# Kernel optimization log

Hardware: AMD Instinct MI355X
Metric: run time of the kernel (lower is better)

## Reference

```python
import jax, jax.numpy as jnp
import numpy as np

N_NODES = 50000
N_EDGES = 800000
T_SEQ = 2048
H = 128  # LSTM hidden size


def _lstm_dir(x, w_ih, w_hh, b, reverse):
    # x: [T, Din]; torch gate order: i, f, g, o
    xg = x @ w_ih.T + b  # [T, 4H] precomputed input contribution
    h0 = jnp.zeros((H,), x.dtype)

    def step(carry, g_t):
        h, c = carry
        g = g_t + h @ w_hh.T
        i, f, gg, o = jnp.split(g, 4)
        i = jax.nn.sigmoid(i); f = jax.nn.sigmoid(f)
        gg = jnp.tanh(gg); o = jax.nn.sigmoid(o)
        c = f * c + i * gg
        h = o * jnp.tanh(c)
        return (h, c), h

    _, hs = jax.lax.scan(step, (h0, h0), xg, reverse=reverse)
    return hs  # [T, H], time-aligned with x


def _bilstm(x, layer_params):
    for (wif, whf, bf, wir, whr, br) in layer_params:
        hf = _lstm_dir(x, wif, whf, bf, reverse=False)
        hr = _lstm_dir(x, wir, whr, br, reverse=True)
        x = jnp.concatenate([hf, hr], axis=-1)
    return x  # [T, 2H]


def _forward(g_mol, feat_seq, edge_src, edge_dst, edge_weight, smiles_kmer,
             w_ih_l0, w_hh_l0, b_ih_l0, b_hh_l0,
             w_ih_l0_r, w_hh_l0_r, b_ih_l0_r, b_hh_l0_r,
             w_ih_l1, w_hh_l1, b_ih_l1, b_hh_l1,
             w_ih_l1_r, w_hh_l1_r, b_ih_l1_r, b_hh_l1_r,
             W1, b1, W2, b2,
             fc1_w, fc1_b, fc2_w, fc2_b, fc3_w, fc3_b, fc4_w, fc4_b):
    n = feat_seq.shape[0]
    # ---- BiLSTM encoder over the (unbatched) molecule sequence [T,17] ----
    layer_params = [
        (w_ih_l0, w_hh_l0, b_ih_l0 + b_hh_l0, w_ih_l0_r, w_hh_l0_r, b_ih_l0_r + b_hh_l0_r),
        (w_ih_l1, w_hh_l1, b_ih_l1 + b_hh_l1, w_ih_l1_r, w_hh_l1_r, b_ih_l1_r + b_hh_l1_r),
    ]
    lstm_out = _bilstm(g_mol, layer_params)              # [T, 256]
    g_mol_vec = lstm_out.mean(axis=0, keepdims=True)     # [1, 256] (mean over dim 0, keepdim)

    # ---- GraphConv 1 (norm='none'): weighted sum-aggregate src->dst, then linear ----
    msg = edge_weight[:, None] * feat_seq[edge_src]                # [E, 128]
    agg = jax.ops.segment_sum(msg, edge_dst, num_segments=n)      # [N, 128]
    h = jax.nn.relu(agg @ W1 + b1)
    # ---- GraphConv 2 ----
    msg2 = edge_weight[:, None] * h[edge_src]                      # [E, 128]
    agg2 = jax.ops.segment_sum(msg2, edge_dst, num_segments=n)    # [N, 128]
    h2 = agg2 @ W2 + b2                                            # [N, 256]
    hg_seq = h2.mean(axis=0, keepdims=True)                        # [1, 256] single-graph mean_nodes

    # ---- concat + MLP head ----
    features = jnp.concatenate([hg_seq, g_mol_vec, smiles_kmer], axis=1)  # [1, 1150]
    out = jax.nn.relu(features @ fc1_w.T + fc1_b)
    out = jax.nn.relu(out @ fc2_w.T + fc2_b)
    out = jax.nn.relu(out @ fc3_w.T + fc3_b)
    out = out @ fc4_w.T + fc4_b
    return out  # [1, 1]


def setup_inputs():
    key = jax.random.key(0)
    ks = iter(jax.random.split(key, 48))

    def rn(shape, s=0.05):
        return jax.random.normal(next(ks), shape, dtype=jnp.float32) * s

    inp = {}
    inp["g_mol"] = jax.random.normal(next(ks), (T_SEQ, 17), dtype=jnp.float32)
    inp["feat_seq"] = jax.random.normal(next(ks), (N_NODES, 128), dtype=jnp.float32)
    inp["edge_src"] = jax.random.randint(next(ks), (N_EDGES,), 0, N_NODES)
    inp["edge_dst"] = jax.random.randint(next(ks), (N_EDGES,), 0, N_NODES)
    inp["edge_weight"] = jax.random.uniform(next(ks), (N_EDGES,), dtype=jnp.float32)
    inp["smiles_kmer"] = jax.random.normal(next(ks), (1, 638), dtype=jnp.float32)
    for l, din in ((0, 17), (1, 2 * H)):
        for suf in ("", "_r"):
            inp[f"w_ih_l{l}{suf}"] = rn((4 * H, din))
            inp[f"w_hh_l{l}{suf}"] = rn((4 * H, H))
            inp[f"b_ih_l{l}{suf}"] = rn((4 * H,))
            inp[f"b_hh_l{l}{suf}"] = rn((4 * H,))
    inp["W1"] = rn((128, 128)); inp["b1"] = jnp.zeros((128,), jnp.float32)
    inp["W2"] = rn((128, 256)); inp["b2"] = jnp.zeros((256,), jnp.float32)
    inp["fc1_w"] = rn((575, 1150)); inp["fc1_b"] = jnp.zeros((575,), jnp.float32)
    inp["fc2_w"] = rn((256, 575)); inp["fc2_b"] = jnp.zeros((256,), jnp.float32)
    inp["fc3_w"] = rn((64, 256)); inp["fc3_b"] = jnp.zeros((64,), jnp.float32)
    inp["fc4_w"] = rn((1, 64)); inp["fc4_b"] = jnp.zeros((1,), jnp.float32)
    return inp


def reference(g_mol, feat_seq, edge_src, edge_dst, edge_weight, smiles_kmer,
              w_ih_l0, w_hh_l0, b_ih_l0, b_hh_l0,
              w_ih_l0_r, w_hh_l0_r, b_ih_l0_r, b_hh_l0_r,
              w_ih_l1, w_hh_l1, b_ih_l1, b_hh_l1,
              w_ih_l1_r, w_hh_l1_r, b_ih_l1_r, b_hh_l1_r,
              W1, b1, W2, b2,
              fc1_w, fc1_b, fc2_w, fc2_b, fc3_w, fc3_b, fc4_w, fc4_b):
    return _forward(g_mol, feat_seq, edge_src, edge_dst, edge_weight, smiles_kmer,
                    w_ih_l0, w_hh_l0, b_ih_l0, b_hh_l0,
                    w_ih_l0_r, w_hh_l0_r, b_ih_l0_r, b_hh_l0_r,
                    w_ih_l1, w_hh_l1, b_ih_l1, b_hh_l1,
                    w_ih_l1_r, w_hh_l1_r, b_ih_l1_r, b_hh_l1_r,
                    W1, b1, W2, b2,
                    fc1_w, fc1_b, fc2_w, fc2_b, fc3_w, fc3_b, fc4_w, fc4_b)
```

## Files before the change

### kernel.cpp

```cpp
#include <hip/hip_runtime.h>
#include <hip/hip_bf16.h>

#define T_SEQ 2048
#define HID 128
#define G4 512
#define N_NODES 50000
#define N_EDGES 800000

typedef float f32x4 __attribute__((ext_vector_type(4)));
typedef _Float16 f16x2 __attribute__((ext_vector_type(2)));
typedef _Float16 f16x8 __attribute__((ext_vector_type(8)));

__device__ __forceinline__ float fast_sigmoid(float x) {
    return 1.0f / (1.0f + __expf(-x));
}
__device__ __forceinline__ float fast_tanh(float x) {
    return 1.0f - 2.0f / (__expf(2.0f * x) + 1.0f);
}

__device__ __forceinline__ float dot2_f16(float bits_w, f16x2 h2, float acc) {
    f16x2 w2 = __builtin_bit_cast(f16x2, bits_w);
#if __has_builtin(__builtin_amdgcn_fdot2)
    return __builtin_amdgcn_fdot2(w2, h2, acc, false);
#else
    asm("v_dot2_f32_f16 %0, %1, %2, %0" : "+v"(acc) : "v"(w2), "v"(h2));
    return acc;
#endif
}

__global__ void xg0_kernel(const float* __restrict__ g_mol,
                           const float* __restrict__ wf, const float* __restrict__ bfi, const float* __restrict__ bfh,
                           const float* __restrict__ wr, const float* __restrict__ bri, const float* __restrict__ brh,
                           float* __restrict__ xg_f, float* __restrict__ xg_r)
{
    int gid = blockIdx.x * blockDim.x + threadIdx.x;
    int j = gid & (G4 - 1);
    int rest = gid >> 9;
    int t = rest & (T_SEQ - 1);
    int dir = rest >> 11;
    const float* w  = dir ? wr  : wf;
    const float* bi = dir ? bri : bfi;
    const float* bh = dir ? brh : bfh;
    float* xg = dir ? xg_r : xg_f;
    const float* x  = g_mol + t * 17;
    const float* wj = w + j * 17;
    float acc = bi[j] + bh[j];
    #pragma unroll
    for (int k = 0; k < 17; ++k) acc += x[k] * wj[k];
    xg[t * G4 + j] = acc;
}

#define EDGE_BLOCKS ((N_EDGES + 1023) / 1024)
__global__ void hist_kernel(const int* __restrict__ esrc, const int* __restrict__ edst,
                            const float* __restrict__ ew,
                            int* __restrict__ cnt, float* __restrict__ outw)
{
    int e = blockIdx.x * 1024 + threadIdx.x;
    if (e < N_EDGES) {
        atomicAdd(&cnt[edst[e]], 1);
        atomicAdd(&outw[esrc[e]], ew[e]);
    }
}

__global__ __launch_bounds__(1024)
void prefix_kernel(const int* __restrict__ cnt, int* __restrict__ offs, int* __restrict__ cursor)
{
    __shared__ int part[1024];
    const int tid = threadIdx.x;
    const int CH = (N_NODES + 1023) / 1024;
    int base = tid * CH;
    int sum = 0;
    for (int i = 0; i < CH; ++i) { int idx = base + i; if (idx < N_NODES) sum += cnt[idx]; }
    part[tid] = sum;
    __syncthreads();
    for (int d = 1; d < 1024; d <<= 1) {
        int v = (tid >= d) ? part[tid - d] : 0;
        __syncthreads();
        part[tid] += v;
        __syncthreads();
    }
    int run = (tid == 0) ? 0 : part[tid - 1];
    for (int i = 0; i < CH; ++i) {
        int idx = base + i;
        if (idx < N_NODES) { offs[idx] = run; cursor[idx] = run; run += cnt[idx]; }
    }
    if (tid == 1023) offs[N_NODES] = run;
}

__global__ void reorder_kernel(const int* __restrict__ esrc, const int* __restrict__ edst,
                               const float* __restrict__ ew, int* __restrict__ cursor,
                               int* __restrict__ csr_src, float* __restrict__ csr_w)
{
    int e = blockIdx.x * 1024 + threadIdx.x;
    if (e < N_EDGES) {
        int pos = atomicAdd(&cursor[edst[e]], 1);
        csr_src[pos] = esrc[e];
        csr_w[pos]   = ew[e];
    }
}

struct ScanSmem {
    _Float16 h16[2][HID] __attribute__((aligned(16)));
    float g[G4];
    float part[G4];
};

#define B8(M) M(0,0,1,2,3) M(1,4,5,6,7) M(2,8,9,10,11) M(3,12,13,14,15) \
              M(4,16,17,18,19) M(5,20,21,22,23) M(6,24,25,26,27) M(7,28,29,30,31)
#define P32(M) M(0) M(1) M(2) M(3) M(4) M(5) M(6) M(7) M(8) M(9) M(10) M(11) \
               M(12) M(13) M(14) M(15) M(16) M(17) M(18) M(19) M(20) M(21) M(22) \
               M(23) M(24) M(25) M(26) M(27) M(28) M(29) M(30) M(31)

__device__ __forceinline__ void lstm_scan_dev(ScanSmem* sm, int dir,
                                              const float* __restrict__ xg,
                                              const float* __restrict__ whh,
                                              float* __restrict__ out,
                                              float* __restrict__ gvec, int write_out)
{
    const int tid = threadIdx.x;
    const int j = tid & (G4 - 1);
    const int half = tid >> 9;

    const float* wptr = whh + j * HID + half * 64;

#define DECL_PK(p) float apk##p; { \
    f16x2 pk_ = { (_Float16)wptr[2*(p)], (_Float16)wptr[2*(p)+1] }; \
    float bits_ = __builtin_bit_cast(float, pk_); \
    asm volatile("v_accvgpr_write_b32 %0, %1" : "=a"(apk##p) : "v"(bits_)); }
    P32(DECL_PK)
#undef DECL_PK

    if (tid < HID) sm->h16[0][tid] = (_Float16)0.0f;
    float c = 0.0f;
    float msum = 0.0f;
    __syncthreads();

    int t0 = dir ? (T_SEQ - 1) : 0;
    float xv = (half == 0) ? xg[t0 * G4 + j] : 0.0f;

    int pp = 0;
    for (int s = 0; s < T_SEQ; ++s) {
        int s2 = (s + 1 < T_SEQ) ? (s + 1) : s;
        int t      = dir ? (T_SEQ - 1 - s)  : s;
        int t_next = dir ? (T_SEQ - 1 - s2) : s2;
        float xv_n = (half == 0) ? xg[t_next * G4 + j] : 0.0f;

        const f16x8* h16v = reinterpret_cast<const f16x8*>(&sm->h16[pp][half * 64]);
        float acc0 = 0.f, acc1 = 0.f, acc2 = 0.f, acc3 = 0.f;
#define DOT_BLK(i, q0, q1, q2, q3) { f16x8 hv = h16v[i]; float b0_, b1_, b2_, b3_; \
        asm volatile("v_accvgpr_read_b32 %0, %1" : "=v"(b0_) : "a"(apk##q0)); \
        asm volatile("v_accvgpr_read_b32 %0, %1" : "=v"(b1_) : "a"(apk##q1)); \
        asm volatile("v_accvgpr_read_b32 %0, %1" : "=v"(b2_) : "a"(apk##q2)); \
        asm volatile("v_accvgpr_read_b32 %0, %1" : "=v"(b3_) : "a"(apk##q3)); \
        f16x2 h0_ = { hv[0], hv[1] }, h1_ = { hv[2], hv[3] }; \
        f16x2 h2_ = { hv[4], hv[5] }, h3_ = { hv[6], hv[7] }; \
        acc0 = dot2_f16(b0_, h0_, acc0); acc1 = dot2_f16(b1_, h1_, acc1); \
        acc2 = dot2_f16(b2_, h2_, acc2); acc3 = dot2_f16(b3_, h3_, acc3); }
        B8(DOT_BLK)
#undef DOT_BLK
        float p = (acc0 + acc1) + (acc2 + acc3);
        if (half) sm->part[j] = p;
        else      sm->g[j] = p + xv;
        __syncthreads();
        if (tid < HID) {
            float ig = fast_sigmoid(sm->g[tid]           + sm->part[tid]);
            float fg = fast_sigmoid(sm->g[HID + tid]     + sm->part[HID + tid]);
            float gg = fast_tanh(   sm->g[2 * HID + tid] + sm->part[2 * HID + tid]);
            float og = fast_sigmoid(sm->g[3 * HID + tid] + sm->part[3 * HID + tid]);
            c = fg * c + ig * gg;
            float hh = og * fast_tanh(c);
            sm->h16[pp ^ 1][tid] = (_Float16)hh;
            if (write_out) out[t * HID + tid] = hh;
            msum += hh;
        }
        __syncthreads();
        pp ^= 1;
        xv = xv_n;
    }
    if (gvec != nullptr && tid < HID) gvec[dir * HID + tid] = msum * (1.0f / (float)T_SEQ);
}

#define GATHER_BLOCKS (N_NODES / 16)
__global__ __launch_bounds__(1024, 1)
void combined1(const float* __restrict__ xg_f, const float* __restrict__ xg_r,
               const float* __restrict__ whh_f, const float* __restrict__ whh_r,
               float* __restrict__ out_f, float* __restrict__ out_r,
               const int* __restrict__ offs, const int* __restrict__ csr_src,
               const float* __restrict__ csr_w, const float* __restrict__ feat,
               float* __restrict__ agg)
{
    __shared__ ScanSmem ssm;
    __shared__ float pad_iso[19456];
    volatile float* vpad = pad_iso;
    vpad[threadIdx.x] = 0.0f;
    int bid = blockIdx.x;
    int tid = threadIdx.x;
    if (bid < 2) {
        lstm_scan_dev(&ssm, bid, bid ? xg_r : xg_f, bid ? whh_r : whh_f,
                      bid ? out_r : out_f, nullptr, 1);
        return;
    }
    int n = (bid - 2) * 16 + (tid >> 6);
    int lane = tid & 63;
    int start = offs[n], end = offs[n + 1];
    float ax = 0.0f, ay = 0.0f;
    const float2* f2 = reinterpret_cast<const float2*>(feat);
    for (int e = start; e < end; ++e) {
        int src = csr_src[e];
        float wgt = csr_w[e];
        float2 v = f2[(long)src * 64 + lane];
        ax += wgt * v.x; ay += wgt * v.y;
    }
    float2 o; o.x = ax; o.y = ay;
    reinterpret_cast<float2*>(agg)[(long)n * 64 + lane] = o;
}

#define XG1_BLOCKS 512
#define NPB2 96
#define G1_BLOCKS ((N_NODES + NPB2 - 1) / NPB2)
__global__ __launch_bounds__(1024, 1)
void combined2(const float* __restrict__ hf0, const float* __restrict__ hr0,
               const float* __restrict__ wf, const float* __restrict__ bfi, const float* __restrict__ bfh,
               const float* __restrict__ wr, const float* __restrict__ bri, const float* __restrict__ brh,
               float* __restrict__ xg_f, float* __restrict__ xg_r,
               const float* __restrict__ W1, const float* __restrict__ b1,
               float* __restrict__ agg)
{
    __shared__ float w_s[128 * 128];
    __shared__ float row_s[8][HID];
    int bid = blockIdx.x;
    int tid = threadIdx.x;
    if (bid < XG1_BLOCKS) {
        int gid = bid * 1024 + tid;
        int j = gid & (G4 - 1);
        int rest = gid >> 9;
        int tb = rest & 511;
        int dir = rest >> 9;
        const float* w  = dir ? wr  : wf;
        const float* bi = dir ? bri : bfi;
        const float* bh = dir ? brh : bfh;
        float* xg = dir ? xg_r : xg_f;
        int t0 = tb * 4;

        float b = bi[j] + bh[j];
        float a0 = b, a1 = b, a2 = b, a3 = b;
        const float4* wrow = reinterpret_cast<const float4*>(w + j * 256);
        const float4* hf = reinterpret_cast<const float4*>(hf0 + t0 * HID);
        const float4* hr = reinterpret_cast<const float4*>(hr0 + t0 * HID);
        #pragma unroll 8
        for (int k = 0; k < 32; ++k) {
            float4 wv = wrow[k];
            float4 v0 = hf[k], v1 = hf[32 + k], v2 = hf[64 + k], v3 = hf[96 + k];
            a0 += wv.x*v0.x + wv.y*v0.y + wv.z*v0.z + wv.w*v0.w;
            a1 += wv.x*v1.x + wv.y*v1.y + wv.z*v1.z + wv.w*v1.w;
            a2 += wv.x*v2.x + wv.y*v2.y + wv.z*v2.z + wv.w*v2.w;
            a3 += wv.x*v3.x + wv.y*v3.y + wv.z*v3.z + wv.w*v3.w;
        }
        #pragma unroll 8
        for (int k = 0; k < 32; ++k) {
            float4 wv = wrow[32 + k];
            float4 v0 = hr[k], v1 = hr[32 + k], v2 = hr[64 + k], v3 = hr[96 + k];
            a0 += wv.x*v0.x + wv.y*v0.y + wv.z*v0.z + wv.w*v0.w;
            a1 += wv.x*v1.x + wv.y*v1.y + wv.z*v1.z + wv.w*v1.w;
            a2 += wv.x*v2.x + wv.y*v2.y + wv.z*v2.z + wv.w*v2.w;
            a3 += wv.x*v3.x + wv.y*v3.y + wv.z*v3.z + wv.w*v3.w;
        }
        xg[(t0 + 0) * G4 + j] = a0;
        xg[(t0 + 1) * G4 + j] = a1;
        xg[(t0 + 2) * G4 + j] = a2;
        xg[(t0 + 3) * G4 + j] = a3;
        return;
    }
    int gb = bid - XG1_BLOCKS;
    int j = tid & 127;
    int sub = tid >> 7;
    for (int i = tid; i < 128 * 128; i += 1024) w_s[i] = W1[i];
    float bj = b1[j];
    __syncthreads();
    int base = gb * NPB2;
    for (int n0 = base; n0 < base + NPB2; n0 += 8) {
        int row = n0 + sub;
        bool valid = row < N_NODES;
        if (valid) row_s[sub][j] = agg[(long)row * HID + j];
        __syncthreads();
        float a = bj;
        #pragma unroll 8
        for (int k = 0; k < 128; ++k) a += row_s[sub][k] * w_s[k * 128 + j];
        __syncthreads();
        if (valid) agg[(long)row * HID + j] = fmaxf(a, 0.0f);
    }
}

#define RED_BLOCKS 512
__global__ __launch_bounds__(1024, 4)
void combined3(const float* __restrict__ xg_f, const float* __restrict__ xg_r,
               const float* __restrict__ whh_f, const float* __restrict__ whh_r,
               float* __restrict__ gvec,
               const float* __restrict__ outw, const float* __restrict__ h,
               float* __restrict__ s_out)
{
    __shared__ ScanSmem ssm;
    __shared__ float red[8 * 128];
    int bid = blockIdx.x;
    int tid = threadIdx.x;
    if (bid < 2) {
        lstm_scan_dev(&ssm, bid, bid ? xg_r : xg_f, bid ? whh_r : whh_f,
                      nullptr, gvec, 0);
        return;
    }
    int hb = bid - 2;
    int f = tid & 127;
    int r = tid >> 7;
    float acc = 0.0f;
    for (int n = hb * 8 + r; n < N_NODES; n += RED_BLOCKS * 8)
        acc += outw[n] * h[(long)n * HID + f];
    red[r * 128 + f] = acc;
    __syncthreads();
    if (tid < 128) {
        float s = 0.0f;
        #pragma unroll
        for (int rr = 0; rr < 8; ++rr) s += red[rr * 128 + tid];
        atomicAdd(&s_out[tid], s);
    }
}

__global__ __launch_bounds__(640)
void head_kernel(const float* __restrict__ s_in, const float* __restrict__ W2, const float* __restrict__ b2,
                 const float* __restrict__ gvec, const float* __restrict__ kmer,
                 const float* __restrict__ fc1w, const float* __restrict__ fc1b,
                 const float* __restrict__ fc2w, const float* __restrict__ fc2b,
                 const float* __restrict__ fc3w, const float* __restrict__ fc3b,
                 const float* __restrict__ fc4w, const float* __restrict__ fc4b,
                 float* __restrict__ out)
{
    __shared__ float feat[1152];
    __shared__ float a1[576];
    __shared__ float a2[256];
    __shared__ float a3[64];
    int tid = threadIdx.x;
    if (tid < 256) {
        float acc = b2[tid];
        const float inv_n = 1.0f / (float)N_NODES;
        for (int k = 0; k < HID; ++k)
            acc += (s_in[k] * inv_n) * W2[k * 256 + tid];
        feat[tid] = acc;
    } else if (tid < 512) {
        feat[tid] = gvec[tid - 256];
    }
    if (tid < 638) feat[512 + tid] = kmer[tid];
    __syncthreads();

    if (tid < 575) {
        const float2* wr = reinterpret_cast<const float2*>(fc1w + (long)tid * 1150);
        const float2* f2 = reinterpret_cast<const float2*>(feat);
        float acc = fc1b[tid];
        for (int k = 0; k < 575; ++k) {
            float2 wv = wr[k]; float2 fv = f2[k];
            acc += wv.x * fv.x + wv.y * fv.y;
        }
        a1[tid] = fmaxf(acc, 0.0f);
    }
    __syncthreads();
    if (tid < 256) {
        const float* wr = fc2w + (long)tid * 575;
        float acc = fc2b[tid];
        for (int k = 0; k < 575; ++k) acc += a1[k] * wr[k];
        a2[tid] = fmaxf(acc, 0.0f);
    }
    __syncthreads();
    if (tid < 64) {
        const float4* wr = reinterpret_cast<const float4*>(fc3w + (long)tid * 256);
        const float4* av4 = reinterpret_cast<const float4*>(a2);
        float acc = fc3b[tid];
        for (int k = 0; k < 64; ++k) {
            float4 wv = wr[k]; float4 av = av4[k];
            acc += wv.x*av.x + wv.y*av.y + wv.z*av.z + wv.w*av.w;
        }
        a3[tid] = fmaxf(acc, 0.0f);
    }
    __syncthreads();
    if (tid == 0) {
        float acc = fc4b[0];
        for (int k = 0; k < 64; ++k) acc += a3[k] * fc4w[k];
        out[0] = acc;
    }
}

extern "C" void kernel_launch(void* const* d_in, const int* in_sizes, int n_in,
                              void* d_out, int out_size, void* d_ws, size_t ws_size,
                              hipStream_t stream)
{
    const float* g_mol = (const float*)d_in[0];
    const float* feat  = (const float*)d_in[1];
    const int*   esrc  = (const int*)d_in[2];
    const int*   edst  = (const int*)d_in[3];
    const float* ew    = (const float*)d_in[4];
    const float* kmer  = (const float*)d_in[5];
    const float* w_ih_l0  = (const float*)d_in[6];
    const float* w_hh_l0  = (const float*)d_in[7];
    const float* b_ih_l0  = (const float*)d_in[8];
    const float* b_hh_l0  = (const float*)d_in[9];
    const float* w_ih_l0r = (const float*)d_in[10];
    const float* w_hh_l0r = (const float*)d_in[11];
    const float* b_ih_l0r = (const float*)d_in[12];
    const float* b_hh_l0r = (const float*)d_in[13];
    const float* w_ih_l1  = (const float*)d_in[14];
    const float* w_hh_l1  = (const float*)d_in[15];
    const float* b_ih_l1  = (const float*)d_in[16];
    const float* b_hh_l1  = (const float*)d_in[17];
    const float* w_ih_l1r = (const float*)d_in[18];
    const float* w_hh_l1r = (const float*)d_in[19];
    const float* b_ih_l1r = (const float*)d_in[20];
    const float* b_hh_l1r = (const float*)d_in[21];
    const float* W1 = (const float*)d_in[22];
    const float* b1 = (const float*)d_in[23];
    const float* W2 = (const float*)d_in[24];
    const float* b2 = (const float*)d_in[25];
    const float* fc1w = (const float*)d_in[26];
    const float* fc1b = (const float*)d_in[27];
    const float* fc2w = (const float*)d_in[28];
    const float* fc2b = (const float*)d_in[29];
    const float* fc3w = (const float*)d_in[30];
    const float* fc3b = (const float*)d_in[31];
    const float* fc4w = (const float*)d_in[32];
    const float* fc4b = (const float*)d_in[33];

    float* ws  = (float*)d_ws;
    float* XGF  = ws;
    float* XGR  = XGF + T_SEQ * G4;
    float* HF0  = XGR + T_SEQ * G4;
    float* HR0  = HF0 + T_SEQ * HID;
    float* GVEC = HR0 + T_SEQ * HID;
    float* SUM  = GVEC + 256;
    float* AGG  = SUM + 128;
    float* OUTW = AGG + (size_t)N_NODES * HID;
    float* CSRW = OUTW + N_NODES;
    int*   CNT  = (int*)(CSRW + N_EDGES);
    int*   OFFS = CNT + (N_NODES + 4);
    int*   CURS = OFFS + (N_NODES + 4);
    int*   CSRS = CURS + (N_NODES + 4);

    hipMemsetAsync(SUM, 0, 128 * sizeof(float), stream);
    hipMemsetAsync(OUTW, 0, N_NODES * sizeof(float), stream);
    hipMemsetAsync(CNT, 0, (N_NODES + 4) * sizeof(int), stream);

    hist_kernel<<<EDGE_BLOCKS, 1024, 0, stream>>>(esrc, edst, ew, CNT, OUTW);
    prefix_kernel<<<1, 1024, 0, stream>>>(CNT, OFFS, CURS);
    reorder_kernel<<<EDGE_BLOCKS, 1024, 0, stream>>>(esrc, edst, ew, CURS, CSRS, CSRW);

    xg0_kernel<<<(2 * T_SEQ * G4) / 256, 256, 0, stream>>>(
        g_mol, w_ih_l0, b_ih_l0, b_hh_l0, w_ih_l0r, b_ih_l0r, b_hh_l0r, XGF, XGR);

    combined1<<<2 + GATHER_BLOCKS, 1024, 0, stream>>>(
        XGF, XGR, w_hh_l0, w_hh_l0r, HF0, HR0, OFFS, CSRS, CSRW, feat, AGG);

    combined2<<<XG1_BLOCKS + G1_BLOCKS, 1024, 0, stream>>>(
        HF0, HR0, w_ih_l1, b_ih_l1, b_hh_l1, w_ih_l1r, b_ih_l1r, b_hh_l1r,
        XGF, XGR, W1, b1, AGG);

    combined3<<<2 + RED_BLOCKS, 1024, 0, stream>>>(
        XGF, XGR, w_hh_l1, w_hh_l1r, GVEC, OUTW, AGG, SUM);

    head_kernel<<<1, 640, 0, stream>>>(SUM, W2, b2, GVEC, kmer,
                                       fc1w, fc1b, fc2w, fc2b, fc3w, fc3b, fc4w, fc4b,
                                       (float*)d_out);
}
```

Measured before the change: 4.589 ms.

## Restructure LSTM scan so each thread owns a full gate row and exchanges via shuffles

New measurement: 5.376 ms. +17.1%, slower.

```diff
diff --git a/kernel.cpp b/kernel.cpp
--- a/kernel.cpp
+++ b/kernel.cpp
@@ -101,15 +101,18 @@
 
 struct ScanSmem {
     _Float16 h16[2][HID] __attribute__((aligned(16)));
-    float g[G4];
-    float part[G4];
 };
 
-#define B8(M) M(0,0,1,2,3) M(1,4,5,6,7) M(2,8,9,10,11) M(3,12,13,14,15) \
-              M(4,16,17,18,19) M(5,20,21,22,23) M(6,24,25,26,27) M(7,28,29,30,31)
-#define P32(M) M(0) M(1) M(2) M(3) M(4) M(5) M(6) M(7) M(8) M(9) M(10) M(11) \
-               M(12) M(13) M(14) M(15) M(16) M(17) M(18) M(19) M(20) M(21) M(22) \
-               M(23) M(24) M(25) M(26) M(27) M(28) M(29) M(30) M(31)
+#define P64(M) M(0) M(1) M(2) M(3) M(4) M(5) M(6) M(7) M(8) M(9) M(10) M(11) \
+               M(12) M(13) M(14) M(15) M(16) M(17) M(18) M(19) M(20) M(21) M(22) M(23) \
+               M(24) M(25) M(26) M(27) M(28) M(29) M(30) M(31) M(32) M(33) M(34) M(35) \
+               M(36) M(37) M(38) M(39) M(40) M(41) M(42) M(43) M(44) M(45) M(46) M(47) \
+               M(48) M(49) M(50) M(51) M(52) M(53) M(54) M(55) M(56) M(57) M(58) M(59) \
+               M(60) M(61) M(62) M(63)
+#define B16(M) M(0,0,1,2,3) M(1,4,5,6,7) M(2,8,9,10,11) M(3,12,13,14,15) \
+               M(4,16,17,18,19) M(5,20,21,22,23) M(6,24,25,26,27) M(7,28,29,30,31) \
+               M(8,32,33,34,35) M(9,36,37,38,39) M(10,40,41,42,43) M(11,44,45,46,47) \
+               M(12,48,49,50,51) M(13,52,53,54,55) M(14,56,57,58,59) M(15,60,61,62,63)
 
 __device__ __forceinline__ void lstm_scan_dev(ScanSmem* sm, int dir,
                                               const float* __restrict__ xg,
@@ -118,16 +121,23 @@
                                               float* __restrict__ gvec, int write_out)
 {
     const int tid = threadIdx.x;
-    const int j = tid & (G4 - 1);
-    const int half = tid >> 9;
-
-    const float* wptr = whh + j * HID + half * 64;
+    if (tid >= 512) {
+        for (int s = 0; s <= T_SEQ; ++s) __syncthreads();
+        return;
+    }
+    const int l = tid & 63;
+    const int w = tid >> 6;
+    const int u = (w << 4) | (l & 15);
+    const int g = l >> 4;
+    const int j = g * HID + u;
+
+    const float* wptr = whh + j * HID;
 
 #define DECL_PK(p) float apk##p; { \
     f16x2 pk_ = { (_Float16)wptr[2*(p)], (_Float16)wptr[2*(p)+1] }; \
     float bits_ = __builtin_bit_cast(float, pk_); \
     asm volatile("v_accvgpr_write_b32 %0, %1" : "=a"(apk##p) : "v"(bits_)); }
-    P32(DECL_PK)
+    P64(DECL_PK)
 #undef DECL_PK
 
     if (tid < HID) sm->h16[0][tid] = (_Float16)0.0f;
@@ -136,16 +146,16 @@
     __syncthreads();
 
     int t0 = dir ? (T_SEQ - 1) : 0;
-    float xv = (half == 0) ? xg[t0 * G4 + j] : 0.0f;
+    float xv = xg[t0 * G4 + j];
 
     int pp = 0;
     for (int s = 0; s < T_SEQ; ++s) {
         int s2 = (s + 1 < T_SEQ) ? (s + 1) : s;
         int t      = dir ? (T_SEQ - 1 - s)  : s;
         int t_next = dir ? (T_SEQ - 1 - s2) : s2;
-        float xv_n = (half == 0) ? xg[t_next * G4 + j] : 0.0f;
-
-        const f16x8* h16v = reinterpret_cast<const f16x8*>(&sm->h16[pp][half * 64]);
+        float xv_n = xg[t_next * G4 + j];
+
+        const f16x8* h16v = reinterpret_cast<const f16x8*>(&sm->h16[pp][0]);
         float acc0 = 0.f, acc1 = 0.f, acc2 = 0.f, acc3 = 0.f;
 #define DOT_BLK(i, q0, q1, q2, q3) { f16x8 hv = h16v[i]; float b0_, b1_, b2_, b3_; \
         asm volatile("v_accvgpr_read_b32 %0, %1" : "=v"(b0_) : "a"(apk##q0)); \
@@ -156,28 +166,36 @@
         f16x2 h2_ = { hv[4], hv[5] }, h3_ = { hv[6], hv[7] }; \
         acc0 = dot2_f16(b0_, h0_, acc0); acc1 = dot2_f16(b1_, h1_, acc1); \
         acc2 = dot2_f16(b2_, h2_, acc2); acc3 = dot2_f16(b3_, h3_, acc3); }
-        B8(DOT_BLK)
+        B16(DOT_BLK)
 #undef DOT_BLK
-        float p = (acc0 + acc1) + (acc2 + acc3);
-        if (half) sm->part[j] = p;
-        else      sm->g[j] = p + xv;
-        __syncthreads();
-        if (tid < HID) {
-            float ig = fast_sigmoid(sm->g[tid]           + sm->part[tid]);
-            float fg = fast_sigmoid(sm->g[HID + tid]     + sm->part[HID + tid]);
-            float gg = fast_tanh(   sm->g[2 * HID + tid] + sm->part[2 * HID + tid]);
-            float og = fast_sigmoid(sm->g[3 * HID + tid] + sm->part[3 * HID + tid]);
-            c = fg * c + ig * gg;
-            float hh = og * fast_tanh(c);
-            sm->h16[pp ^ 1][tid] = (_Float16)hh;
-            if (write_out) out[t * HID + tid] = hh;
+        float p = (acc0 + acc1) + (acc2 + acc3) + xv;
+
+        float v1 = __shfl_xor(p, 16, 64);
+        float v2 = __shfl_xor(p, 32, 64);
+        float v3 = __shfl_xor(p, 48, 64);
+        float gi, gf, gg_, go;
+        {
+            int s0 = g;            gi  = s0 == 0 ? p : s0 == 1 ? v1 : s0 == 2 ? v2 : v3;
+            int s1 = g ^ 1;        gf  = s1 == 0 ? p : s1 == 1 ? v1 : s1 == 2 ? v2 : v3;
+            int s2_ = g ^ 2;       gg_ = s2_ == 0 ? p : s2_ == 1 ? v1 : s2_ == 2 ? v2 : v3;
+            int s3 = g ^ 3;        go  = s3 == 0 ? p : s3 == 1 ? v1 : s3 == 2 ? v2 : v3;
+        }
+        float ig = fast_sigmoid(gi);
+        float fg = fast_sigmoid(gf);
+        float gt = fast_tanh(gg_);
+        float og = fast_sigmoid(go);
+        c = fg * c + ig * gt;
+        float hh = og * fast_tanh(c);
+        if (g == 0) {
+            sm->h16[pp ^ 1][u] = (_Float16)hh;
+            if (write_out) out[t * HID + u] = hh;
             msum += hh;
         }
         __syncthreads();
         pp ^= 1;
         xv = xv_n;
     }
-    if (gvec != nullptr && tid < HID) gvec[dir * HID + tid] = msum * (1.0f / (float)T_SEQ);
+    if (gvec != nullptr && g == 0) gvec[dir * HID + u] = msum * (1.0f / (float)T_SEQ);
 }
 
 #define GATHER_BLOCKS (N_NODES / 16)
@@ -190,7 +208,7 @@
                float* __restrict__ agg)
 {
     __shared__ ScanSmem ssm;
-    __shared__ float pad_iso[19456];
+    __shared__ float pad_iso[20480];
     volatile float* vpad = pad_iso;
     vpad[threadIdx.x] = 0.0f;
     int bid = blockIdx.x;
```

## Overlap layer-1 LSTM scan with GraphConv1 linear and fused weighted reduction

Applied to the files above, without the earlier changes.

Measured after the change: 4.466 ms. -2.7%, faster.

```diff
diff --git a/kernel.cpp b/kernel.cpp
--- a/kernel.cpp
+++ b/kernel.cpp
@@ -28,12 +28,27 @@
 #endif
 }
 
-__global__ void xg0_kernel(const float* __restrict__ g_mol,
-                           const float* __restrict__ wf, const float* __restrict__ bfi, const float* __restrict__ bfh,
-                           const float* __restrict__ wr, const float* __restrict__ bri, const float* __restrict__ brh,
-                           float* __restrict__ xg_f, float* __restrict__ xg_r)
-{
-    int gid = blockIdx.x * blockDim.x + threadIdx.x;
+#define HIST_BLOCKS ((N_EDGES + 1023) / 1024)
+#define XG0_BLOCKS ((2 * T_SEQ * G4) / 1024)
+__global__ void fused0_kernel(const int* __restrict__ esrc, const int* __restrict__ edst,
+                              const float* __restrict__ ew,
+                              int* __restrict__ cnt, float* __restrict__ outw,
+                              const float* __restrict__ g_mol,
+                              const float* __restrict__ wf, const float* __restrict__ bfi, const float* __restrict__ bfh,
+                              const float* __restrict__ wr, const float* __restrict__ bri, const float* __restrict__ brh,
+                              float* __restrict__ xg_f, float* __restrict__ xg_r)
+{
+    int bid = blockIdx.x;
+    int tid = threadIdx.x;
+    if (bid < HIST_BLOCKS) {
+        int e = bid * 1024 + tid;
+        if (e < N_EDGES) {
+            atomicAdd(&cnt[edst[e]], 1);
+            atomicAdd(&outw[esrc[e]], ew[e]);
+        }
+        return;
+    }
+    int gid = (bid - HIST_BLOCKS) * 1024 + tid;
     int j = gid & (G4 - 1);
     int rest = gid >> 9;
     int t = rest & (T_SEQ - 1);
@@ -50,18 +65,6 @@
     xg[t * G4 + j] = acc;
 }
 
-#define EDGE_BLOCKS ((N_EDGES + 1023) / 1024)
-__global__ void hist_kernel(const int* __restrict__ esrc, const int* __restrict__ edst,
-                            const float* __restrict__ ew,
-                            int* __restrict__ cnt, float* __restrict__ outw)
-{
-    int e = blockIdx.x * 1024 + threadIdx.x;
-    if (e < N_EDGES) {
-        atomicAdd(&cnt[edst[e]], 1);
-        atomicAdd(&outw[esrc[e]], ew[e]);
-    }
-}
-
 __global__ __launch_bounds__(1024)
 void prefix_kernel(const int* __restrict__ cnt, int* __restrict__ offs, int* __restrict__ cursor)
 {
@@ -97,6 +100,52 @@
         csr_src[pos] = esrc[e];
         csr_w[pos]   = ew[e];
     }
+}
+
+#define XG1_BLOCKS 512
+__global__ void xg1_kernel(const float* __restrict__ hf0, const float* __restrict__ hr0,
+                           const float* __restrict__ wf, const float* __restrict__ bfi, const float* __restrict__ bfh,
+                           const float* __restrict__ wr, const float* __restrict__ bri, const float* __restrict__ brh,
+                           float* __restrict__ xg_f, float* __restrict__ xg_r)
+{
+    int gid = blockIdx.x * 1024 + threadIdx.x;
+    int j = gid & (G4 - 1);
+    int rest = gid >> 9;
+    int tb = rest & 511;
+    int dir = rest >> 9;
+    const float* w  = dir ? wr  : wf;
+    const float* bi = dir ? bri : bfi;
+    const float* bh = dir ? brh : bfh;
+    float* xg = dir ? xg_r : xg_f;
+    int t0 = tb * 4;
+
+    float b = bi[j] + bh[j];
+    float a0 = b, a1 = b, a2 = b, a3 = b;
+    const float4* wrow = reinterpret_cast<const float4*>(w + j * 256);
+    const float4* hf = reinterpret_cast<const float4*>(hf0 + t0 * HID);
+    const float4* hr = reinterpret_cast<const float4*>(hr0 + t0 * HID);
+    #pragma unroll 8
+    for (int k = 0; k < 32; ++k) {
+        float4 wv = wrow[k];
+        float4 v0 = hf[k], v1 = hf[32 + k], v2 = hf[64 + k], v3 = hf[96 + k];
+        a0 += wv.x*v0.x + wv.y*v0.y + wv.z*v0.z + wv.w*v0.w;
+        a1 += wv.x*v1.x + wv.y*v1.y + wv.z*v1.z + wv.w*v1.w;
+        a2 += wv.x*v2.x + wv.y*v2.y + wv.z*v2.z + wv.w*v2.w;
+        a3 += wv.x*v3.x + wv.y*v3.y + wv.z*v3.z + wv.w*v3.w;
+    }
+    #pragma unroll 8
+    for (int k = 0; k < 32; ++k) {
+        float4 wv = wrow[32 + k];
+        float4 v0 = hr[k], v1 = hr[32 + k], v2 = hr[64 + k], v3 = hr[96 + k];
+        a0 += wv.x*v0.x + wv.y*v0.y + wv.z*v0.z + wv.w*v0.w;
+        a1 += wv.x*v1.x + wv.y*v1.y + wv.z*v1.z + wv.w*v1.w;
+        a2 += wv.x*v2.x + wv.y*v2.y + wv.z*v2.z + wv.w*v2.w;
+        a3 += wv.x*v3.x + wv.y*v3.y + wv.z*v3.z + wv.w*v3.w;
+    }
+    xg[(t0 + 0) * G4 + j] = a0;
+    xg[(t0 + 1) * G4 + j] = a1;
+    xg[(t0 + 2) * G4 + j] = a2;
+    xg[(t0 + 3) * G4 + j] = a3;
 }
 
 struct ScanSmem {
@@ -215,92 +264,23 @@
     reinterpret_cast<float2*>(agg)[(long)n * 64 + lane] = o;
 }
 
-#define XG1_BLOCKS 512
 #define NPB2 96
 #define G1_BLOCKS ((N_NODES + NPB2 - 1) / NPB2)
 __global__ __launch_bounds__(1024, 1)
-void combined2(const float* __restrict__ hf0, const float* __restrict__ hr0,
-               const float* __restrict__ wf, const float* __restrict__ bfi, const float* __restrict__ bfh,
-               const float* __restrict__ wr, const float* __restrict__ bri, const float* __restrict__ brh,
-               float* __restrict__ xg_f, float* __restrict__ xg_r,
-               const float* __restrict__ W1, const float* __restrict__ b1,
-               float* __restrict__ agg)
-{
-    __shared__ float w_s[128 * 128];
-    __shared__ float row_s[8][HID];
-    int bid = blockIdx.x;
-    int tid = threadIdx.x;
-    if (bid < XG1_BLOCKS) {
-        int gid = bid * 1024 + tid;
-        int j = gid & (G4 - 1);
-        int rest = gid >> 9;
-        int tb = rest & 511;
-        int dir = rest >> 9;
-        const float* w  = dir ? wr  : wf;
-        const float* bi = dir ? bri : bfi;
-        const float* bh = dir ? brh : bfh;
-        float* xg = dir ? xg_r : xg_f;
-        int t0 = tb * 4;
-
-        float b = bi[j] + bh[j];
-        float a0 = b, a1 = b, a2 = b, a3 = b;
-        const float4* wrow = reinterpret_cast<const float4*>(w + j * 256);
-        const float4* hf = reinterpret_cast<const float4*>(hf0 + t0 * HID);
-        const float4* hr = reinterpret_cast<const float4*>(hr0 + t0 * HID);
-        #pragma unroll 8
-        for (int k = 0; k < 32; ++k) {
-            float4 wv = wrow[k];
-            float4 v0 = hf[k], v1 = hf[32 + k], v2 = hf[64 + k], v3 = hf[96 + k];
-            a0 += wv.x*v0.x + wv.y*v0.y + wv.z*v0.z + wv.w*v0.w;
-            a1 += wv.x*v1.x + wv.y*v1.y + wv.z*v1.z + wv.w*v1.w;
-            a2 += wv.x*v2.x + wv.y*v2.y + wv.z*v2.z + wv.w*v2.w;
-            a3 += wv.x*v3.x + wv.y*v3.y + wv.z*v3.z + wv.w*v3.w;
-        }
-        #pragma unroll 8
-        for (int k = 0; k < 32; ++k) {
-            float4 wv = wrow[32 + k];
-            float4 v0 = hr[k], v1 = hr[32 + k], v2 = hr[64 + k], v3 = hr[96 + k];
-            a0 += wv.x*v0.x + wv.y*v0.y + wv.z*v0.z + wv.w*v0.w;
-            a1 += wv.x*v1.x + wv.y*v1.y + wv.z*v1.z + wv.w*v1.w;
-            a2 += wv.x*v2.x + wv.y*v2.y + wv.z*v2.z + wv.w*v2.w;
-            a3 += wv.x*v3.x + wv.y*v3.y + wv.z*v3.z + wv.w*v3.w;
-        }
-        xg[(t0 + 0) * G4 + j] = a0;
-        xg[(t0 + 1) * G4 + j] = a1;
-        xg[(t0 + 2) * G4 + j] = a2;
-        xg[(t0 + 3) * G4 + j] = a3;
-        return;
-    }
-    int gb = bid - XG1_BLOCKS;
-    int j = tid & 127;
-    int sub = tid >> 7;
-    for (int i = tid; i < 128 * 128; i += 1024) w_s[i] = W1[i];
-    float bj = b1[j];
-    __syncthreads();
-    int base = gb * NPB2;
-    for (int n0 = base; n0 < base + NPB2; n0 += 8) {
-        int row = n0 + sub;
-        bool valid = row < N_NODES;
-        if (valid) row_s[sub][j] = agg[(long)row * HID + j];
-        __syncthreads();
-        float a = bj;
-        #pragma unroll 8
-        for (int k = 0; k < 128; ++k) a += row_s[sub][k] * w_s[k * 128 + j];
-        __syncthreads();
-        if (valid) agg[(long)row * HID + j] = fmaxf(a, 0.0f);
-    }
-}
-
-#define RED_BLOCKS 512
-__global__ __launch_bounds__(1024, 4)
 void combined3(const float* __restrict__ xg_f, const float* __restrict__ xg_r,
                const float* __restrict__ whh_f, const float* __restrict__ whh_r,
                float* __restrict__ gvec,
-               const float* __restrict__ outw, const float* __restrict__ h,
+               const float* __restrict__ W1, const float* __restrict__ b1,
+               const float* __restrict__ agg, const float* __restrict__ outw,
                float* __restrict__ s_out)
 {
     __shared__ ScanSmem ssm;
-    __shared__ float red[8 * 128];
+    __shared__ float w_s[128 * 128];
+    __shared__ float row_s[8][HID];
+    __shared__ float red[8][HID];
+    __shared__ float pad_iso[2048];
+    volatile float* vpad = pad_iso;
+    vpad[threadIdx.x & 2047] = 0.0f;
     int bid = blockIdx.x;
     int tid = threadIdx.x;
     if (bid < 2) {
@@ -308,18 +288,31 @@
                       nullptr, gvec, 0);
         return;
     }
-    int hb = bid - 2;
-    int f = tid & 127;
-    int r = tid >> 7;
-    float acc = 0.0f;
-    for (int n = hb * 8 + r; n < N_NODES; n += RED_BLOCKS * 8)
-        acc += outw[n] * h[(long)n * HID + f];
-    red[r * 128 + f] = acc;
+    int gb = bid - 2;
+    int j = tid & 127;
+    int sub = tid >> 7;
+    for (int i = tid; i < 128 * 128; i += 1024) w_s[i] = W1[i];
+    float bj = b1[j];
+    float sacc = 0.0f;
+    __syncthreads();
+    int base = gb * NPB2;
+    for (int n0 = base; n0 < base + NPB2; n0 += 8) {
+        int row = n0 + sub;
+        bool valid = row < N_NODES;
+        if (valid) row_s[sub][j] = agg[(long)row * HID + j];
+        __syncthreads();
+        float a = bj;
+        #pragma unroll 8
+        for (int k = 0; k < 128; ++k) a += row_s[sub][k] * w_s[k * 128 + j];
+        __syncthreads();
+        if (valid) sacc += outw[row] * fmaxf(a, 0.0f);
+    }
+    red[sub][j] = sacc;
     __syncthreads();
     if (tid < 128) {
         float s = 0.0f;
         #pragma unroll
-        for (int rr = 0; rr < 8; ++rr) s += red[rr * 128 + tid];
+        for (int rr = 0; rr < 8; ++rr) s += red[rr][tid];
         atomicAdd(&s_out[tid], s);
     }
 }
@@ -444,22 +437,20 @@
     hipMemsetAsync(OUTW, 0, N_NODES * sizeof(float), stream);
     hipMemsetAsync(CNT, 0, (N_NODES + 4) * sizeof(int), stream);
 
-    hist_kernel<<<EDGE_BLOCKS, 1024, 0, stream>>>(esrc, edst, ew, CNT, OUTW);
+    fused0_kernel<<<HIST_BLOCKS + XG0_BLOCKS, 1024, 0, stream>>>(
+        esrc, edst, ew, CNT, OUTW,
+        g_mol, w_ih_l0, b_ih_l0, b_hh_l0, w_ih_l0r, b_ih_l0r, b_hh_l0r, XGF, XGR);
     prefix_kernel<<<1, 1024, 0, stream>>>(CNT, OFFS, CURS);
-    reorder_kernel<<<EDGE_BLOCKS, 1024, 0, stream>>>(esrc, edst, ew, CURS, CSRS, CSRW);
-
-    xg0_kernel<<<(2 * T_SEQ * G4) / 256, 256, 0, stream>>>(
-        g_mol, w_ih_l0, b_ih_l0, b_hh_l0, w_ih_l0r, b_ih_l0r, b_hh_l0r, XGF, XGR);
+    reorder_kernel<<<HIST_BLOCKS, 1024, 0, stream>>>(esrc, edst, ew, CURS, CSRS, CSRW);
 
     combined1<<<2 + GATHER_BLOCKS, 1024, 0, stream>>>(
         XGF, XGR, w_hh_l0, w_hh_l0r, HF0, HR0, OFFS, CSRS, CSRW, feat, AGG);
 
-    combined2<<<XG1_BLOCKS + G1_BLOCKS, 1024, 0, stream>>>(
-        HF0, HR0, w_ih_l1, b_ih_l1, b_hh_l1, w_ih_l1r, b_ih_l1r, b_hh_l1r,
-        XGF, XGR, W1, b1, AGG);
-
-    combined3<<<2 + RED_BLOCKS, 1024, 0, stream>>>(
-        XGF, XGR, w_hh_l1, w_hh_l1r, GVEC, OUTW, AGG, SUM);
+    xg1_kernel<<<XG1_BLOCKS, 1024, 0, stream>>>(
+        HF0, HR0, w_ih_l1, b_ih_l1, b_hh_l1, w_ih_l1r, b_ih_l1r, b_hh_l1r, XGF, XGR);
+
+    combined3<<<2 + G1_BLOCKS, 1024, 0, stream>>>(
+        XGF, XGR, w_hh_l1, w_hh_l1r, GVEC, W1, b1, AGG, OUTW, SUM);
 
     head_kernel<<<1, 640, 0, stream>>>(SUM, W2, b2, GVEC, kmer,
                                        fc1w, fc1b, fc2w, fc2b, fc3w, fc3b, fc4w, fc4b,
```
